# Kernel tuning notes

Measured on AMD Instinct MI355X. Metric: run time of the kernel, lower is better.

Reference implementation:

```python
import jax, jax.numpy as jnp
import numpy as np

B, C, N = 4, 3, 1024
D = H = W = 32

def setup_inputs() -> dict:
    key = jax.random.key(0)
    k1, k2 = jax.random.split(key)
    xyz = jax.random.normal(k1, (B, C, N), dtype=jnp.float32)
    grid = jax.random.uniform(k2, (C, D, H, W), dtype=jnp.float32)
    s1 = jnp.ones((1,), dtype=jnp.float32)
    s2 = jnp.ones((1,), dtype=jnp.float32)
    return {"xyz": xyz, "grid": grid, "s1": s1, "s2": s2}

def reference(xyz, grid, s1, s2):
    # dist[b,d,h,w,n] = sum_c (xyz[b,c,n] - grid[c,d,h,w])^2
    x2 = jnp.sum(xyz * xyz, axis=1)            # (B, N)
    g2 = jnp.sum(grid * grid, axis=0)          # (D, H, W)
    xg = jnp.einsum('bcn,cdhw->bdhwn', xyz, grid)  # (B, D, H, W, N)
    dist = x2[:, None, None, None, :] + g2[None, :, :, :, None] - 2.0 * xg
    v = jnp.abs(s2[0]) * jnp.exp(-jnp.abs(s1[0]) * dist)   # (B, D, H, W, N)
    v = jax.nn.softmax(v, axis=4)
    p, _ = jax.lax.top_k(v, 2)                 # top-2 over last axis (N)
    return p[..., 0] - p[..., 1]               # (B, D, H, W) top-2 margin
```

## Files before the change

### kernel.cpp

```cpp
#include <hip/hip_runtime.h>
#include <math.h>


#define LOG2E 1.44269504088896340736f

__global__ __launch_bounds__(256, 2) void p2v_kernel(
    const float* __restrict__ xyz,
    const float* __restrict__ grid,
    const float* __restrict__ s1,
    const float* __restrict__ s2,
    float* __restrict__ out)
{
    __shared__ float4 A[1024];

    const int tid = threadIdx.x;
    const int b   = blockIdx.x >> 7;
    const int dhw = ((blockIdx.x & 127) << 8) + tid;

    const float s1a = fabsf(s1[0]);
    const float s2a = fabsf(s2[0]);
    const float c1  = LOG2E * s1a;
    const float Ls2 = LOG2E * s2a;

    const float* xb = xyz + b * 3072;
    #pragma unroll
    for (int i = 0; i < 4; ++i) {
        const int n = tid + i * 256;
        const float x = xb[n], y = xb[1024 + n], z = xb[2048 + n];
        const float x2 = fmaf(x, x, fmaf(y, y, z * z));
        A[n] = make_float4(-c1 * x2, 2.f * c1 * x, 2.f * c1 * y, 2.f * c1 * z);
    }
    __syncthreads();

    const float g0 = grid[dhw];
    const float g1 = grid[32768 + dhw];
    const float g2 = grid[65536 + dhw];
    const float Ct  = s2a * __builtin_amdgcn_exp2f(-c1 * fmaf(g0, g0, fmaf(g1, g1, g2 * g2)));
    const float ECt = LOG2E * Ct;

    float t0 = -INFINITY, t1 = -INFINITY;
    float S0 = 0.f, S1 = 0.f, S2 = 0.f, S3 = 0.f;

    for (int n0 = 0; n0 < 1024; n0 += 8) {
        float4 r[8];
        #pragma unroll
        for (int j = 0; j < 8; ++j) r[j] = A[n0 + j];
        #pragma unroll
        for (int j = 0; j < 8; ++j) {
            const float4 a = r[j];
            const float q = fmaf(g0, a.y, fmaf(g1, a.z, fmaf(g2, a.w, a.x)));
            t1 = __builtin_amdgcn_fmed3f(t0, t1, q);
            t0 = fmaxf(t0, q);
            const float w = __builtin_amdgcn_exp2f(
                fmaf(ECt, __builtin_amdgcn_exp2f(q), -Ls2));
            if (j == 0) S0 += w; else if (j == 1) S1 += w;
            else if (j == 2) S2 += w; else if (j == 3) S3 += w;
            else if (j == 4) S0 += w; else if (j == 5) S1 += w;
            else if (j == 6) S2 += w; else S3 += w;
        }
    }
    const float S = (S0 + S1) + (S2 + S3);

    const float u0 = __builtin_amdgcn_exp2f(t0);
    const float u1 = __builtin_amdgcn_exp2f(t1);
    const float w0 = __builtin_amdgcn_exp2f(fmaf(ECt, u0, -Ls2));
    const float num = w0 * (1.f - __builtin_amdgcn_exp2f(ECt * (u1 - u0)));
    out[b * 32768 + dhw] = num / S;
}

extern "C" void kernel_launch(void* const* d_in, const int* in_sizes, int n_in,
                              void* d_out, int out_size, void* d_ws, size_t ws_size,
                              hipStream_t stream) {
    const float* xyz  = (const float*)d_in[0];
    const float* grid = (const float*)d_in[1];
    const float* s1   = (const float*)d_in[2];
    const float* s2   = (const float*)d_in[3];
    float* out        = (float*)d_out;
    hipLaunchKernelGGL(p2v_kernel, dim3(512), dim3(256), 0, stream,
                       xyz, grid, s1, s2, out);
}
```

Measured before the change: 99.98 us.

## Precompute point table in separate kernel and read it via uniform global loads

```diff
diff --git a/kernel.cpp b/kernel.cpp
--- a/kernel.cpp
+++ b/kernel.cpp
@@ -4,15 +4,25 @@
 
 #define LOG2E 1.44269504088896340736f
 
+__global__ void build_tab(const float* __restrict__ xyz,
+                          const float* __restrict__ s1,
+                          float4* __restrict__ tab) {
+    const int i = blockIdx.x * 256 + threadIdx.x;
+    const int b = i >> 10, n = i & 1023;
+    const float c1 = LOG2E * fabsf(s1[0]);
+    const float* xb = xyz + b * 3072;
+    const float x = xb[n], y = xb[1024 + n], z = xb[2048 + n];
+    const float x2 = fmaf(x, x, fmaf(y, y, z * z));
+    tab[i] = make_float4(-c1 * x2, 2.f * c1 * x, 2.f * c1 * y, 2.f * c1 * z);
+}
+
 __global__ __launch_bounds__(256, 2) void p2v_kernel(
-    const float* __restrict__ xyz,
+    const float4* __restrict__ tab,
     const float* __restrict__ grid,
     const float* __restrict__ s1,
     const float* __restrict__ s2,
     float* __restrict__ out)
 {
-    __shared__ float4 A[1024];
-
     const int tid = threadIdx.x;
     const int b   = blockIdx.x >> 7;
     const int dhw = ((blockIdx.x & 127) << 8) + tid;
@@ -22,44 +32,33 @@
     const float c1  = LOG2E * s1a;
     const float Ls2 = LOG2E * s2a;
 
-    const float* xb = xyz + b * 3072;
-    #pragma unroll
-    for (int i = 0; i < 4; ++i) {
-        const int n = tid + i * 256;
-        const float x = xb[n], y = xb[1024 + n], z = xb[2048 + n];
-        const float x2 = fmaf(x, x, fmaf(y, y, z * z));
-        A[n] = make_float4(-c1 * x2, 2.f * c1 * x, 2.f * c1 * y, 2.f * c1 * z);
-    }
-    __syncthreads();
-
     const float g0 = grid[dhw];
     const float g1 = grid[32768 + dhw];
     const float g2 = grid[65536 + dhw];
     const float Ct  = s2a * __builtin_amdgcn_exp2f(-c1 * fmaf(g0, g0, fmaf(g1, g1, g2 * g2)));
     const float ECt = LOG2E * Ct;
 
+    const float4* tb = tab + (b << 10);
+
     float t0 = -INFINITY, t1 = -INFINITY;
-    float S0 = 0.f, S1 = 0.f, S2 = 0.f, S3 = 0.f;
+    float Sa0 = 0.f, Sa1 = 0.f, Sa2 = 0.f, Sa3 = 0.f;
 
-    for (int n0 = 0; n0 < 1024; n0 += 8) {
-        float4 r[8];
+    for (int n0 = 0; n0 < 1024; n0 += 16) {
         #pragma unroll
-        for (int j = 0; j < 8; ++j) r[j] = A[n0 + j];
-        #pragma unroll
-        for (int j = 0; j < 8; ++j) {
-            const float4 a = r[j];
+        for (int j = 0; j < 16; ++j) {
+            const float4 a = tb[n0 + j];
             const float q = fmaf(g0, a.y, fmaf(g1, a.z, fmaf(g2, a.w, a.x)));
             t1 = __builtin_amdgcn_fmed3f(t0, t1, q);
             t0 = fmaxf(t0, q);
             const float w = __builtin_amdgcn_exp2f(
                 fmaf(ECt, __builtin_amdgcn_exp2f(q), -Ls2));
-            if (j == 0) S0 += w; else if (j == 1) S1 += w;
-            else if (j == 2) S2 += w; else if (j == 3) S3 += w;
-            else if (j == 4) S0 += w; else if (j == 5) S1 += w;
-            else if (j == 6) S2 += w; else S3 += w;
+            if ((j & 3) == 0) Sa0 += w;
+            else if ((j & 3) == 1) Sa1 += w;
+            else if ((j & 3) == 2) Sa2 += w;
+            else Sa3 += w;
         }
     }
-    const float S = (S0 + S1) + (S2 + S3);
+    const float S = (Sa0 + Sa1) + (Sa2 + Sa3);
 
     const float u0 = __builtin_amdgcn_exp2f(t0);
     const float u1 = __builtin_amdgcn_exp2f(t1);
@@ -76,6 +75,9 @@
     const float* s1   = (const float*)d_in[2];
     const float* s2   = (const float*)d_in[3];
     float* out        = (float*)d_out;
+    float4* tab       = (float4*)d_ws;
+
+    hipLaunchKernelGGL(build_tab, dim3(16), dim3(256), 0, stream, xyz, s1, tab);
     hipLaunchKernelGGL(p2v_kernel, dim3(512), dim3(256), 0, stream,
-                       xyz, grid, s1, s2, out);
+                       tab, grid, s1, s2, out);
 }
```

Measured after the change: 114.8 us. 14.8% more time.

## Compute two grid voxels per thread to reuse shared-memory point loads

Applied to the files above, without the earlier changes.

```diff
diff --git a/kernel.cpp b/kernel.cpp
--- a/kernel.cpp
+++ b/kernel.cpp
@@ -4,7 +4,7 @@
 
 #define LOG2E 1.44269504088896340736f
 
-__global__ __launch_bounds__(256, 2) void p2v_kernel(
+__global__ __launch_bounds__(256, 1) void p2v_kernel(
     const float* __restrict__ xyz,
     const float* __restrict__ grid,
     const float* __restrict__ s1,
@@ -13,9 +13,10 @@
 {
     __shared__ float4 A[1024];
 
-    const int tid = threadIdx.x;
-    const int b   = blockIdx.x >> 7;
-    const int dhw = ((blockIdx.x & 127) << 8) + tid;
+    const int tid  = threadIdx.x;
+    const int b    = blockIdx.x >> 6;
+    const int dhw0 = ((blockIdx.x & 63) << 9) + tid;
+    const int dhw1 = dhw0 + 256;
 
     const float s1a = fabsf(s1[0]);
     const float s2a = fabsf(s2[0]);
@@ -32,14 +33,16 @@
     }
     __syncthreads();
 
-    const float g0 = grid[dhw];
-    const float g1 = grid[32768 + dhw];
-    const float g2 = grid[65536 + dhw];
-    const float Ct  = s2a * __builtin_amdgcn_exp2f(-c1 * fmaf(g0, g0, fmaf(g1, g1, g2 * g2)));
-    const float ECt = LOG2E * Ct;
+    const float ga0 = grid[dhw0], ga1 = grid[32768 + dhw0], ga2 = grid[65536 + dhw0];
+    const float gb0 = grid[dhw1], gb1 = grid[32768 + dhw1], gb2 = grid[65536 + dhw1];
+    const float ECa = LOG2E * s2a *
+        __builtin_amdgcn_exp2f(-c1 * fmaf(ga0, ga0, fmaf(ga1, ga1, ga2 * ga2)));
+    const float ECb = LOG2E * s2a *
+        __builtin_amdgcn_exp2f(-c1 * fmaf(gb0, gb0, fmaf(gb1, gb1, gb2 * gb2)));
 
-    float t0 = -INFINITY, t1 = -INFINITY;
-    float S0 = 0.f, S1 = 0.f, S2 = 0.f, S3 = 0.f;
+    float t0aE = -INFINITY, t1aE = -INFINITY, t0aO = -INFINITY, t1aO = -INFINITY;
+    float t0bE = -INFINITY, t1bE = -INFINITY, t0bO = -INFINITY, t1bO = -INFINITY;
+    float SaE = 0.f, SaO = 0.f, SbE = 0.f, SbO = 0.f;
 
     for (int n0 = 0; n0 < 1024; n0 += 8) {
         float4 r[8];
@@ -48,24 +51,44 @@
         #pragma unroll
         for (int j = 0; j < 8; ++j) {
             const float4 a = r[j];
-            const float q = fmaf(g0, a.y, fmaf(g1, a.z, fmaf(g2, a.w, a.x)));
-            t1 = __builtin_amdgcn_fmed3f(t0, t1, q);
-            t0 = fmaxf(t0, q);
-            const float w = __builtin_amdgcn_exp2f(
-                fmaf(ECt, __builtin_amdgcn_exp2f(q), -Ls2));
-            if (j == 0) S0 += w; else if (j == 1) S1 += w;
-            else if (j == 2) S2 += w; else if (j == 3) S3 += w;
-            else if (j == 4) S0 += w; else if (j == 5) S1 += w;
-            else if (j == 6) S2 += w; else S3 += w;
+            const float qa = fmaf(ga0, a.y, fmaf(ga1, a.z, fmaf(ga2, a.w, a.x)));
+            const float qb = fmaf(gb0, a.y, fmaf(gb1, a.z, fmaf(gb2, a.w, a.x)));
+            if (j & 1) {
+                t1aO = __builtin_amdgcn_fmed3f(t0aO, t1aO, qa); t0aO = fmaxf(t0aO, qa);
+                t1bO = __builtin_amdgcn_fmed3f(t0bO, t1bO, qb); t0bO = fmaxf(t0bO, qb);
+            } else {
+                t1aE = __builtin_amdgcn_fmed3f(t0aE, t1aE, qa); t0aE = fmaxf(t0aE, qa);
+                t1bE = __builtin_amdgcn_fmed3f(t0bE, t1bE, qb); t0bE = fmaxf(t0bE, qb);
+            }
+            const float wa = __builtin_amdgcn_exp2f(
+                fmaf(ECa, __builtin_amdgcn_exp2f(qa), -Ls2));
+            const float wb = __builtin_amdgcn_exp2f(
+                fmaf(ECb, __builtin_amdgcn_exp2f(qb), -Ls2));
+            if (j & 1) { SaO += wa; SbO += wb; }
+            else       { SaE += wa; SbE += wb; }
         }
     }
-    const float S = (S0 + S1) + (S2 + S3);
 
-    const float u0 = __builtin_amdgcn_exp2f(t0);
-    const float u1 = __builtin_amdgcn_exp2f(t1);
-    const float w0 = __builtin_amdgcn_exp2f(fmaf(ECt, u0, -Ls2));
-    const float num = w0 * (1.f - __builtin_amdgcn_exp2f(ECt * (u1 - u0)));
-    out[b * 32768 + dhw] = num / S;
+    const float t0a = fmaxf(t0aE, t0aO);
+    const float t1a = fmaxf(fminf(t0aE, t0aO), fmaxf(t1aE, t1aO));
+    const float t0b = fmaxf(t0bE, t0bO);
+    const float t1b = fmaxf(fminf(t0bE, t0bO), fmaxf(t1bE, t1bO));
+    const float Sa = SaE + SaO;
+    const float Sb = SbE + SbO;
+
+    const float u0a = __builtin_amdgcn_exp2f(t0a);
+    const float u1a = __builtin_amdgcn_exp2f(t1a);
+    const float w0a = __builtin_amdgcn_exp2f(fmaf(ECa, u0a, -Ls2));
+    const float numa = w0a * (1.f - __builtin_amdgcn_exp2f(ECa * (u1a - u0a)));
+
+    const float u0b = __builtin_amdgcn_exp2f(t0b);
+    const float u1b = __builtin_amdgcn_exp2f(t1b);
+    const float w0b = __builtin_amdgcn_exp2f(fmaf(ECb, u0b, -Ls2));
+    const float numb = w0b * (1.f - __builtin_amdgcn_exp2f(ECb * (u1b - u0b)));
+
+    float* ob = out + b * 32768;
+    ob[dhw0] = numa / Sa;
+    ob[dhw1] = numb / Sb;
 }
 
 extern "C" void kernel_launch(void* const* d_in, const int* in_sizes, int n_in,
@@ -76,6 +99,6 @@
     const float* s1   = (const float*)d_in[2];
     const float* s2   = (const float*)d_in[3];
     float* out        = (float*)d_out;
-    hipLaunchKernelGGL(p2v_kernel, dim3(512), dim3(256), 0, stream,
+    hipLaunchKernelGGL(p2v_kernel, dim3(256), dim3(256), 0, stream,
                        xyz, grid, s1, s2, out);
 }
```

Result: slower. 105.5 us (+5.6%).

## Split each voxel's N-reduction across four lanes with shuffle merge of top-2 and sum

Applied to the files above, without the earlier changes.

```diff
diff --git a/kernel.cpp b/kernel.cpp
--- a/kernel.cpp
+++ b/kernel.cpp
@@ -4,7 +4,7 @@
 
 #define LOG2E 1.44269504088896340736f
 
-__global__ __launch_bounds__(256, 2) void p2v_kernel(
+__global__ __launch_bounds__(256, 8) void p2v_kernel(
     const float* __restrict__ xyz,
     const float* __restrict__ grid,
     const float* __restrict__ s1,
@@ -14,8 +14,10 @@
     __shared__ float4 A[1024];
 
     const int tid = threadIdx.x;
-    const int b   = blockIdx.x >> 7;
-    const int dhw = ((blockIdx.x & 127) << 8) + tid;
+    const int b   = blockIdx.x >> 9;
+    const int k   = blockIdx.x & 511;
+    const int dhw = (k << 6) + (tid >> 2);
+    const int c   = tid & 3;
 
     const float s1a = fabsf(s1[0]);
     const float s2a = fabsf(s2[0]);
@@ -35,37 +37,50 @@
     const float g0 = grid[dhw];
     const float g1 = grid[32768 + dhw];
     const float g2 = grid[65536 + dhw];
-    const float Ct  = s2a * __builtin_amdgcn_exp2f(-c1 * fmaf(g0, g0, fmaf(g1, g1, g2 * g2)));
-    const float ECt = LOG2E * Ct;
+    const float EC = LOG2E * s2a *
+        __builtin_amdgcn_exp2f(-c1 * fmaf(g0, g0, fmaf(g1, g1, g2 * g2)));
 
-    float t0 = -INFINITY, t1 = -INFINITY;
-    float S0 = 0.f, S1 = 0.f, S2 = 0.f, S3 = 0.f;
+    float t0E = -INFINITY, t1E = -INFINITY, t0O = -INFINITY, t1O = -INFINITY;
+    float S0 = 0.f, S1 = 0.f;
 
-    for (int n0 = 0; n0 < 1024; n0 += 8) {
-        float4 r[8];
-        #pragma unroll
-        for (int j = 0; j < 8; ++j) r[j] = A[n0 + j];
-        #pragma unroll
-        for (int j = 0; j < 8; ++j) {
-            const float4 a = r[j];
-            const float q = fmaf(g0, a.y, fmaf(g1, a.z, fmaf(g2, a.w, a.x)));
-            t1 = __builtin_amdgcn_fmed3f(t0, t1, q);
-            t0 = fmaxf(t0, q);
-            const float w = __builtin_amdgcn_exp2f(
-                fmaf(ECt, __builtin_amdgcn_exp2f(q), -Ls2));
-            if (j == 0) S0 += w; else if (j == 1) S1 += w;
-            else if (j == 2) S2 += w; else if (j == 3) S3 += w;
-            else if (j == 4) S0 += w; else if (j == 5) S1 += w;
-            else if (j == 6) S2 += w; else S3 += w;
+    const float4* Ac = A + c;
+    #pragma unroll 8
+    for (int i = 0; i < 256; ++i) {
+        const float4 a = Ac[i << 2];
+        const float q = fmaf(g0, a.y, fmaf(g1, a.z, fmaf(g2, a.w, a.x)));
+        if (i & 1) {
+            t1O = __builtin_amdgcn_fmed3f(t0O, t1O, q);
+            t0O = fmaxf(t0O, q);
+        } else {
+            t1E = __builtin_amdgcn_fmed3f(t0E, t1E, q);
+            t0E = fmaxf(t0E, q);
         }
+        const float w = __builtin_amdgcn_exp2f(
+            fmaf(EC, __builtin_amdgcn_exp2f(q), -Ls2));
+        if (i & 1) S1 += w; else S0 += w;
     }
-    const float S = (S0 + S1) + (S2 + S3);
 
-    const float u0 = __builtin_amdgcn_exp2f(t0);
-    const float u1 = __builtin_amdgcn_exp2f(t1);
-    const float w0 = __builtin_amdgcn_exp2f(fmaf(ECt, u0, -Ls2));
-    const float num = w0 * (1.f - __builtin_amdgcn_exp2f(ECt * (u1 - u0)));
-    out[b * 32768 + dhw] = num / S;
+    float t0 = fmaxf(t0E, t0O);
+    float t1 = fmaxf(fminf(t0E, t0O), fmaxf(t1E, t1O));
+    float S  = S0 + S1;
+
+    #pragma unroll
+    for (int m = 1; m <= 2; m <<= 1) {
+        const float ot0 = __shfl_xor(t0, m);
+        const float ot1 = __shfl_xor(t1, m);
+        const float oS  = __shfl_xor(S, m);
+        t1 = fmaxf(fminf(t0, ot0), fmaxf(t1, ot1));
+        t0 = fmaxf(t0, ot0);
+        S += oS;
+    }
+
+    if (c == 0) {
+        const float u0 = __builtin_amdgcn_exp2f(t0);
+        const float u1 = __builtin_amdgcn_exp2f(t1);
+        const float w0 = __builtin_amdgcn_exp2f(fmaf(EC, u0, -Ls2));
+        const float num = w0 * (1.f - __builtin_amdgcn_exp2f(EC * (u1 - u0)));
+        out[b * 32768 + dhw] = num / S;
+    }
 }
 
 extern "C" void kernel_launch(void* const* d_in, const int* in_sizes, int n_in,
@@ -76,6 +91,6 @@
     const float* s1   = (const float*)d_in[2];
     const float* s2   = (const float*)d_in[3];
     float* out        = (float*)d_out;
-    hipLaunchKernelGGL(p2v_kernel, dim3(512), dim3(256), 0, stream,
+    hipLaunchKernelGGL(p2v_kernel, dim3(2048), dim3(256), 0, stream,
                        xyz, grid, s1, s2, out);
 }
```

Measured after the change: 97.54 us. 2.4% less time.
